# Optimization experiments

Measured on AMD Instinct MI355X. Metric: run time of the kernel, lower is better.

## Reference

```python
import jax, jax.numpy as jnp
import numpy as np

HEADS = 8
DIM_HEAD = 32
EPS = 1e-5


def setup_inputs() -> dict:
    key = jax.random.key(0)
    ks = jax.random.split(key, 12)
    b, dim, H, W = 16, 256, 64, 64
    led = 128
    hid = HEADS * DIM_HEAD
    return {
        "x": jax.random.normal(ks[0], (b, dim, H, W), dtype=jnp.float32),
        "condition": jax.random.normal(ks[1], (b, led), dtype=jnp.float32),
        "w_qkv": jax.random.normal(ks[2], (3 * hid, dim), dtype=jnp.float32) * 0.02,
        "w_lk": jax.random.normal(ks[3], (hid, led), dtype=jnp.float32) * 0.02,
        "b_lk": jax.random.normal(ks[4], (hid,), dtype=jnp.float32) * 0.02,
        "w_lq": jax.random.normal(ks[5], (hid, led), dtype=jnp.float32) * 0.02,
        "b_lq": jax.random.normal(ks[6], (hid,), dtype=jnp.float32) * 0.02,
        "w_out": jax.random.normal(ks[7], (dim, hid), dtype=jnp.float32) * 0.02,
        "b_out": jax.random.normal(ks[8], (dim,), dtype=jnp.float32) * 0.02,
        "gn_gamma": jnp.ones((dim,), dtype=jnp.float32),
        "gn_beta": jnp.zeros((dim,), dtype=jnp.float32),
    }


def reference(x, condition, w_qkv, w_lk, b_lk, w_lq, b_lq, w_out, b_out, gn_gamma, gn_beta):
    b, c, H, W = x.shape
    n = H * W
    scale = DIM_HEAD ** (-0.5)
    hid = HEADS * DIM_HEAD

    # 1x1 conv QKV projection (no bias)
    qkv = jnp.einsum('oc,bchw->bohw', w_qkv, x)  # [b, 3*hid, H, W]
    qkv = qkv.reshape(b, 3, HEADS, DIM_HEAD, n)
    q, k, v = qkv[:, 0], qkv[:, 1], qkv[:, 2]     # each [b, heads, d, n]

    # conditioning biases
    lk = (condition @ w_lk.T + b_lk).reshape(b, HEADS, DIM_HEAD, 1)
    lq = (condition @ w_lq.T + b_lq).reshape(b, HEADS, DIM_HEAD, 1)
    k = k + lk
    q = q + lq

    # double softmax (linear attention)
    q = jax.nn.softmax(q, axis=-2) * scale  # over feature dim d
    k = jax.nn.softmax(k, axis=-1)          # over spatial dim n

    context = jnp.einsum('bhdn,bhen->bhde', k, v)   # [b, h, d, e]
    out = jnp.einsum('bhde,bhdn->bhen', context, q)  # [b, h, e, n]
    out = out.reshape(b, hid, H, W)

    # to_out: 1x1 conv + bias, then GroupNorm(1, dim)
    y = jnp.einsum('oc,bchw->bohw', w_out, out) + b_out[None, :, None, None]
    mean = jnp.mean(y, axis=(1, 2, 3), keepdims=True)
    var = jnp.var(y, axis=(1, 2, 3), keepdims=True)
    y = (y - mean) * jax.lax.rsqrt(var + EPS)
    return y * gn_gamma[None, :, None, None] + gn_beta[None, :, None, None]
```

## Files before the change

kernel.cpp:

```cpp
#include <hip/hip_runtime.h>


#define NB    16
#define DIM   256
#define NSP   4096
#define LED   128
#define HID   256
#define NHEAD 8
#define SCALE 0.17677669529663687f

typedef __bf16 bf16x8 __attribute__((ext_vector_type(8)));
typedef float f32x4 __attribute__((ext_vector_type(4)));
typedef unsigned short us8 __attribute__((ext_vector_type(8)));
typedef unsigned short us4 __attribute__((ext_vector_type(4)));

__device__ __forceinline__ unsigned short f2bf(float f){
  unsigned u = __builtin_bit_cast(unsigned, f);
  u += 0x7fffu + ((u >> 16) & 1u);
  return (unsigned short)(u >> 16);
}
__device__ __forceinline__ float bf2f(unsigned short h){
  unsigned u = ((unsigned)h) << 16;
  return __builtin_bit_cast(float, u);
}
__device__ __forceinline__ bf16x8 ldb8(const unsigned short* p){
  us8 r = *(const us8*)p;
  return __builtin_bit_cast(bf16x8, r);
}
__device__ __forceinline__ f32x4 mfma16(bf16x8 a, bf16x8 b, f32x4 c){
  return __builtin_amdgcn_mfma_f32_16x16x32_bf16(a, b, c, 0, 0, 0);
}
__device__ __forceinline__ void gl16(const unsigned short* g, unsigned short* l){
  __builtin_amdgcn_global_load_lds(
      (const __attribute__((address_space(1))) unsigned int*)g,
      (__attribute__((address_space(3))) unsigned int*)l,
      16, 0, 0);
}

__global__ __launch_bounds__(256) void k0_prep(
    const float* __restrict__ wqkv, const float* __restrict__ cond,
    const float* __restrict__ wlk, const float* __restrict__ blk,
    const float* __restrict__ wlq, const float* __restrict__ blq,
    unsigned short* __restrict__ whi,
    float* __restrict__ lk, float* __restrict__ lq)
{
  const int idx = blockIdx.x*256 + threadIdx.x;
  if (idx < 768*256){
    whi[idx] = f2bf(wqkv[idx]);
  } else {
    int i = idx - 768*256;
    const int which = (i >= NB*HID) ? 1 : 0;
    i &= (NB*HID - 1);
    const int b = i >> 8, o = i & 255;
    const float* wm = which ? wlq : wlk;
    const float* bs = which ? blq : blk;
    float s = bs[o];
    const float* c = cond + b*LED;
    const float* wr = wm + o*LED;
    for (int j=0;j<LED;j++) s += c[j]*wr[j];
    (which ? lq : lk)[i] = s;
  }
}

__global__ __launch_bounds__(256) void k1_txpose(
    const float* __restrict__ x, unsigned short* __restrict__ xt)
{
  __shared__ float tile[64][65];
  const int c0 = blockIdx.x*64, n0 = blockIdx.y*64, b = blockIdx.z;
  const int t = threadIdx.x;
  const int tr = t >> 6, tc = t & 63;
  const float* xp = x + ((size_t)b*DIM + c0)*NSP + n0;
  #pragma unroll
  for (int i=0;i<16;i++){
    const int cl = i*4 + tr;
    tile[cl][tc] = xp[(size_t)cl*NSP + tc];
  }
  __syncthreads();
  unsigned short* xtp = xt + ((size_t)b*NSP + n0)*DIM + c0;
  #pragma unroll
  for (int i=0;i<16;i++){
    const int nl = i*4 + tr;
    xtp[(size_t)nl*DIM + tc] = f2bf(tile[tc][nl]);
  }
}

__global__ __launch_bounds__(256) void k2_gemm1(
    const unsigned short* __restrict__ whi,
    const unsigned short* __restrict__ xt,
    const float* __restrict__ lkv, const float* __restrict__ lqv,
    unsigned short* __restrict__ qh,
    unsigned short* __restrict__ kexp, unsigned short* __restrict__ vout,
    float* __restrict__ ksum)
{
  __shared__ __align__(16) unsigned char smraw[34816];
  unsigned short* Ah  = (unsigned short*)smraw;
  unsigned short* Bt  = (unsigned short*)(smraw + 16384);
  unsigned short* stg = (unsigned short*)smraw;

  const int nt = blockIdx.x, mt = blockIdx.y, b = blockIdx.z;
  const int o0 = mt*128, n0 = nt*128;
  const int t = threadIdx.x, lane = t & 63, wv = t >> 6;
  const int wr = wv >> 1, wc = wv & 1;
  const int cl = lane & 15, g = lane >> 4;

  f32x4 acc[4][4];
  const f32x4 z4 = {0.f,0.f,0.f,0.f};
  #pragma unroll
  for (int m=0;m<4;m++)
    #pragma unroll
    for (int n=0;n<4;n++) acc[m][n] = z4;

  const unsigned short* xb = xt + ((size_t)b*NSP + n0)*DIM;
  const int rowc = lane >> 3;
  const int gcol = 8*((lane & 7) ^ rowc);

  for (int kt=0; kt<4; kt++){
    const int k0 = kt*64;
    __syncthreads();
    #pragma unroll
    for (int j=0;j<4;j++){
      const int rg = wv*4 + j;
      const int rr = rg*8 + rowc;
      gl16(&whi[(size_t)(o0+rr)*DIM + k0 + gcol], &Ah[rg*512]);
      gl16(&xb [(size_t)rr*DIM      + k0 + gcol], &Bt[rg*512]);
    }
    __syncthreads();
    #pragma unroll
    for (int kk=0; kk<2; kk++){
      const int ko = kk*32 + g*8;
      const int kosw = ko ^ ((cl & 7) << 3);
      bf16x8 a1[4], bb[4];
      #pragma unroll
      for (int m=0;m<4;m++){
        const int row = wr*64 + m*16 + cl;
        a1[m] = ldb8(&Ah[row*64 + kosw]);
      }
      #pragma unroll
      for (int n=0;n<4;n++){
        const int row = wc*64 + n*16 + cl;
        bb[n] = ldb8(&Bt[row*64 + kosw]);
      }
      #pragma unroll
      for (int m=0;m<4;m++)
        #pragma unroll
        for (int n=0;n<4;n++)
          acc[m][n] = mfma16(a1[m], bb[n], acc[m][n]);
    }
  }

  __syncthreads();

  if (mt < 2){
    float lqr[4][4];
    #pragma unroll
    for (int m=0;m<4;m++)
      #pragma unroll
      for (int i=0;i<4;i++)
        lqr[m][i] = lqv[b*HID + o0 + wr*64 + m*16 + g*4 + i];
    #pragma unroll
    for (int j=0;j<2;j++){
      #pragma unroll
      for (int nf=0;nf<4;nf++){
        float e[8]; float mx = -1e30f;
        #pragma unroll
        for (int mm=0;mm<2;mm++)
          #pragma unroll
          for (int i=0;i<4;i++){
            const int m = 2*j+mm;
            const float v = acc[m][nf][i] + lqr[m][i];
            e[mm*4+i] = v; mx = fmaxf(mx, v);
          }
        mx = fmaxf(mx, __shfl_xor(mx, 16));
        mx = fmaxf(mx, __shfl_xor(mx, 32));
        float s = 0.f;
        #pragma unroll
        for (int q2=0;q2<8;q2++){ e[q2] = __expf(e[q2]-mx); s += e[q2]; }
        s += __shfl_xor(s, 16);
        s += __shfl_xor(s, 32);
        const float r = 1.f/s;
        const int n_local = wc*64 + nf*16 + cl;
        #pragma unroll
        for (int mm=0;mm<2;mm++){
          const int dg_local = wr*64 + (2*j+mm)*16 + g*4;
          us4 h4;
          #pragma unroll
          for (int i=0;i<4;i++) h4[i] = f2bf(e[mm*4+i]*r);
          *(us4*)&stg[n_local*136 + dg_local] = h4;
        }
      }
    }
    __syncthreads();
    unsigned short* qbase = qh + ((size_t)b*NSP + n0)*HID + o0;
    #pragma unroll
    for (int i2=0;i2<8;i2++){
      const int n_local = wv*32 + i2*4 + (lane>>4);
      const int dg8 = (lane&15)*8;
      us8 val = *(const us8*)&stg[n_local*136 + dg8];
      *(us8*)&qbase[(size_t)n_local*HID + dg8] = val;
    }
  } else {
    const int isK = (mt < 4);
    const int dgbase = isK ? (mt-2)*128 : (mt-4)*128;
    #pragma unroll
    for (int m=0;m<4;m++)
      #pragma unroll
      for (int i=0;i<4;i++){
        const int dg_local = wr*64 + m*16 + g*4 + i;
        const int nb0 = wc*64 + cl;
        if (isK){
          const float lkval = lkv[b*HID + dgbase + dg_local];
          float s = 0.f;
          #pragma unroll
          for (int nf=0;nf<4;nf++){
            const float v = __expf(acc[m][nf][i] + lkval);
            const unsigned short hh = f2bf(v);
            stg[dg_local*136 + nb0 + nf*16] = hh;
            s += bf2f(hh);
          }
          s += __shfl_xor(s,1); s += __shfl_xor(s,2);
          s += __shfl_xor(s,4); s += __shfl_xor(s,8);
          if (cl == 0) atomicAdd(&ksum[b*HID + dgbase + dg_local], s);
        } else {
          #pragma unroll
          for (int nf=0;nf<4;nf++)
            stg[dg_local*136 + nb0 + nf*16] = f2bf(acc[m][nf][i]);
        }
      }
    __syncthreads();
    unsigned short* obase = (isK ? kexp : vout) + ((size_t)b*HID + dgbase)*NSP + n0;
    #pragma unroll
    for (int i2=0;i2<8;i2++){
      const int dg_local = wv*32 + i2*4 + (lane>>4);
      const int n8 = (lane&15)*8;
      us8 val = *(const us8*)&stg[dg_local*136 + n8];
      *(us8*)&obase[(size_t)dg_local*NSP + n8] = val;
    }
  }
}

__global__ __launch_bounds__(256) void k3_ctx(
    const unsigned short* __restrict__ kexp, const unsigned short* __restrict__ vv,
    float* __restrict__ ctxp)
{
  const int half = blockIdx.x, h = blockIdx.y, b = blockIdx.z;
  const int t = threadIdx.x, lane = t&63, wv = t>>6;
  const int cl = lane&15, g = lane>>4;
  const int nstart = half*2048 + wv*512;
  f32x4 acc[2][2];
  const f32x4 z4 = {0.f,0.f,0.f,0.f};
  acc[0][0]=z4; acc[0][1]=z4; acc[1][0]=z4; acc[1][1]=z4;
  const unsigned short* kb = kexp + ((size_t)b*HID + h*32)*NSP;
  const unsigned short* vb = vv   + ((size_t)b*HID + h*32)*NSP;
  for (int ks=0; ks<16; ks++){
    const int k = nstart + ks*32 + g*8;
    bf16x8 a0 = ldb8(&kb[(size_t)(cl)   *NSP + k]);
    bf16x8 a1 = ldb8(&kb[(size_t)(16+cl)*NSP + k]);
    bf16x8 b0 = ldb8(&vb[(size_t)(cl)   *NSP + k]);
    bf16x8 b1 = ldb8(&vb[(size_t)(16+cl)*NSP + k]);
    acc[0][0] = mfma16(a0,b0,acc[0][0]);
    acc[0][1] = mfma16(a0,b1,acc[0][1]);
    acc[1][0] = mfma16(a1,b0,acc[1][0]);
    acc[1][1] = mfma16(a1,b1,acc[1][1]);
  }
  float* outp = ctxp + ((((size_t)b*NHEAD + h)*2 + half)*4 + wv)*1024;
  #pragma unroll
  for (int dm=0;dm<2;dm++)
    #pragma unroll
    for (int em=0;em<2;em++)
      #pragma unroll
      for (int i=0;i<4;i++)
        outp[(dm*16 + g*4 + i)*32 + em*16 + cl] = acc[dm][em][i];
}

__global__ __launch_bounds__(256) void k4_m(
    const float* __restrict__ ctxp, const float* __restrict__ ksum,
    const float* __restrict__ wout,
    unsigned short* __restrict__ mhi, unsigned short* __restrict__ mlo)
{
  const int h = blockIdx.x, b = blockIdx.y;
  __shared__ float ctxl[32][32];
  __shared__ float rkn[32];
  const int t = threadIdx.x;
  const float* base = ctxp + (((size_t)b*NHEAD + h)*8)*1024;
  #pragma unroll
  for (int r=0;r<4;r++){
    const int de = r*256 + t;
    float s = 0.f;
    #pragma unroll
    for (int p=0;p<8;p++) s += base[p*1024 + de];
    ctxl[de>>5][de&31] = s;
  }
  if (t < 32) rkn[t] = SCALE / ksum[b*HID + h*32 + t];
  __syncthreads();
  float w[32];
  const float* wrow = wout + (size_t)t*HID + h*32;
  #pragma unroll
  for (int el=0;el<32;el++) w[el] = wrow[el];
  for (int dl=0; dl<32; dl++){
    float s = 0.f;
    #pragma unroll
    for (int el=0;el<32;el++) s += w[el]*ctxl[dl][el];
    s *= rkn[dl];
    const unsigned short hh = f2bf(s);
    const size_t off = ((size_t)b*HID + t)*HID + h*32 + dl;
    mhi[off] = hh;
    mlo[off] = f2bf(s - bf2f(hh));
  }
}

__global__ __launch_bounds__(256) void k5a_stats(
    const unsigned short* __restrict__ mhi,
    const unsigned short* __restrict__ qhp, const float* __restrict__ bout,
    float* __restrict__ bsum, float* __restrict__ bssq)
{
  __shared__ __align__(16) unsigned char smraw[32768];
  unsigned short* Ah = (unsigned short*)smraw;
  unsigned short* Bh = (unsigned short*)(smraw + 16384);
  __shared__ float red[8];

  const int nt = blockIdx.x, mt = blockIdx.y, b = blockIdx.z;
  const int o0 = mt*128, n0 = nt*128;
  const int t = threadIdx.x, lane = t&63, wv = t>>6;
  const int wr = wv>>1, wc = wv&1;
  const int cl = lane&15, g = lane>>4;

  f32x4 acc[4][4];
  const f32x4 z4 = {0.f,0.f,0.f,0.f};
  #pragma unroll
  for (int m=0;m<4;m++)
    #pragma unroll
    for (int n=0;n<4;n++) acc[m][n] = z4;

  const unsigned short* ab_h = mhi + (size_t)b*HID*HID;
  const unsigned short* bb_h = qhp + ((size_t)b*NSP + n0)*HID;
  const int rowc = lane >> 3;
  const int gcol = 8*((lane & 7) ^ rowc);

  for (int kt=0; kt<4; kt++){
    const int k0 = kt*64;
    __syncthreads();
    #pragma unroll
    for (int j=0;j<4;j++){
      const int rg = wv*4 + j;
      const int rr = rg*8 + rowc;
      gl16(&ab_h[(size_t)(o0+rr)*HID + k0 + gcol], &Ah[rg*512]);
      gl16(&bb_h[(size_t)rr*HID      + k0 + gcol], &Bh[rg*512]);
    }
    __syncthreads();
    #pragma unroll
    for (int kk=0;kk<2;kk++){
      const int ko = kk*32 + g*8;
      const int kosw = ko ^ ((cl & 7) << 3);
      bf16x8 ah[4], bh[4];
      #pragma unroll
      for (int m=0;m<4;m++)
        ah[m] = ldb8(&Ah[(wr*64 + m*16 + cl)*64 + kosw]);
      #pragma unroll
      for (int n=0;n<4;n++)
        bh[n] = ldb8(&Bh[(wc*64 + n*16 + cl)*64 + kosw]);
      #pragma unroll
      for (int m=0;m<4;m++)
        #pragma unroll
        for (int n=0;n<4;n++)
          acc[m][n] = mfma16(ah[m], bh[n], acc[m][n]);
    }
  }

  float lsum = 0.f, lss = 0.f;
  #pragma unroll
  for (int m=0;m<4;m++)
    #pragma unroll
    for (int i=0;i<4;i++){
      const float bo = bout[o0 + wr*64 + m*16 + g*4 + i];
      #pragma unroll
      for (int nf=0;nf<4;nf++){
        const float v = acc[m][nf][i] + bo;
        lsum += v; lss += v*v;
      }
    }
  #pragma unroll
  for (int sft=1; sft<64; sft<<=1){
    lsum += __shfl_xor(lsum, sft);
    lss  += __shfl_xor(lss,  sft);
  }
  if (lane == 0){ red[wv] = lsum; red[4+wv] = lss; }
  __syncthreads();
  if (t == 0){
    atomicAdd(&bsum[b], red[0]+red[1]+red[2]+red[3]);
    atomicAdd(&bssq[b], red[4]+red[5]+red[6]+red[7]);
  }
}

__global__ __launch_bounds__(256) void k5b_write(
    const unsigned short* __restrict__ mhi, const unsigned short* __restrict__ mlo,
    const unsigned short* __restrict__ qhp, const float* __restrict__ bout,
    const float* __restrict__ bsum, const float* __restrict__ bssq,
    const float* __restrict__ gamma, const float* __restrict__ beta,
    float* __restrict__ out)
{
  __shared__ __align__(16) unsigned char smraw[49152];
  unsigned short* Ah = (unsigned short*)smraw;
  unsigned short* Al = (unsigned short*)(smraw + 16384);
  unsigned short* Bh = (unsigned short*)(smraw + 32768);
  float* stg = (float*)smraw;

  const int nt = blockIdx.x, mt = blockIdx.y, b = blockIdx.z;
  const int o0 = mt*128, n0 = nt*128;
  const int t = threadIdx.x, lane = t&63, wv = t>>6;
  const int wr = wv>>1, wc = wv&1;
  const int cl = lane&15, g = lane>>4;

  f32x4 acc[4][4];
  const f32x4 z4 = {0.f,0.f,0.f,0.f};
  #pragma unroll
  for (int m=0;m<4;m++)
    #pragma unroll
    for (int n=0;n<4;n++) acc[m][n] = z4;

  const unsigned short* ab_h = mhi + (size_t)b*HID*HID;
  const unsigned short* ab_l = mlo + (size_t)b*HID*HID;
  const unsigned short* bb_h = qhp + ((size_t)b*NSP + n0)*HID;
  const int rowc = lane >> 3;
  const int gcol = 8*((lane & 7) ^ rowc);

  for (int kt=0; kt<4; kt++){
    const int k0 = kt*64;
    __syncthreads();
    #pragma unroll
    for (int j=0;j<4;j++){
      const int rg = wv*4 + j;
      const int rr = rg*8 + rowc;
      gl16(&ab_h[(size_t)(o0+rr)*HID + k0 + gcol], &Ah[rg*512]);
      gl16(&ab_l[(size_t)(o0+rr)*HID + k0 + gcol], &Al[rg*512]);
      gl16(&bb_h[(size_t)rr*HID      + k0 + gcol], &Bh[rg*512]);
    }
    __syncthreads();
    #pragma unroll
    for (int kk=0;kk<2;kk++){
      const int ko = kk*32 + g*8;
      const int kosw = ko ^ ((cl & 7) << 3);
      bf16x8 ah[4], al[4], bh[4];
      #pragma unroll
      for (int m=0;m<4;m++){
        const int row = wr*64 + m*16 + cl;
        ah[m] = ldb8(&Ah[row*64 + kosw]);
        al[m] = ldb8(&Al[row*64 + kosw]);
      }
      #pragma unroll
      for (int n=0;n<4;n++){
        const int row = wc*64 + n*16 + cl;
        bh[n] = ldb8(&Bh[row*64 + kosw]);
      }
      #pragma unroll
      for (int m=0;m<4;m++)
        #pragma unroll
        for (int n=0;n<4;n++){
          acc[m][n] = mfma16(ah[m], bh[n], acc[m][n]);
          acc[m][n] = mfma16(al[m], bh[n], acc[m][n]);
        }
    }
  }

  const float inv = 1.f/1048576.f;
  const float mean = bsum[b]*inv;
  const float var  = bssq[b]*inv - mean*mean;
  const float ri = rsqrtf(var + 1e-5f);
  float gav[4][4], bev[4][4];
  #pragma unroll
  for (int m=0;m<4;m++)
    #pragma unroll
    for (int i=0;i<4;i++){
      const int o = o0 + wr*64 + m*16 + g*4 + i;
      const float ga = gamma[o]*ri;
      gav[m][i] = ga;
      bev[m][i] = beta[o] + (bout[o]-mean)*ga;
    }

  #pragma unroll
  for (int p=0;p<2;p++){
    __syncthreads();
    #pragma unroll
    for (int mm=0;mm<2;mm++){
      const int m = 2*p+mm;
      #pragma unroll
      for (int nf=0;nf<4;nf++)
        #pragma unroll
        for (int i=0;i<4;i++){
          const int lr = wr*32 + mm*16 + g*4 + i;
          stg[lr*132 + wc*64 + nf*16 + cl] = acc[m][nf][i]*gav[m][i] + bev[m][i];
        }
    }
    __syncthreads();
    #pragma unroll
    for (int i2=0;i2<8;i2++){
      const int lr = wv*16 + i2*2 + (lane>>5);
      const int colw = (lane&31)*4;
      f32x4 v = *(const f32x4*)&stg[lr*132 + colw];
      const int dg = o0 + (lr>>5)*64 + p*32 + (lr&31);
      *(f32x4*)&out[((size_t)b*HID + dg)*NSP + n0 + colw] = v;
    }
  }
}

#define OFF_XT     0ull
#define OFF_QH     33554432ull
#define OFF_CTXP   100663296ull
#define OFF_MH     104857600ull
#define OFF_ML     106954752ull
#define OFF_LK     109051904ull
#define OFF_LQ     109068288ull
#define OFF_WHI    109084672ull
#define OFF_KSUM   109871104ull
#define OFF_BSUM   109887488ull
#define OFF_BSSQ   109887552ull

extern "C" void kernel_launch(void* const* d_in, const int* in_sizes, int n_in,
                              void* d_out, int out_size, void* d_ws, size_t ws_size,
                              hipStream_t stream) {
  const float* x     = (const float*)d_in[0];
  const float* cond  = (const float*)d_in[1];
  const float* wqkv  = (const float*)d_in[2];
  const float* wlk   = (const float*)d_in[3];
  const float* blk   = (const float*)d_in[4];
  const float* wlq   = (const float*)d_in[5];
  const float* blq   = (const float*)d_in[6];
  const float* wout  = (const float*)d_in[7];
  const float* bout  = (const float*)d_in[8];
  const float* gamma = (const float*)d_in[9];
  const float* beta  = (const float*)d_in[10];

  char* ws = (char*)d_ws;
  unsigned short* xt   = (unsigned short*)(ws + OFF_XT);
  unsigned short* qh   = (unsigned short*)(ws + OFF_QH);
  float*          ctxp = (float*)(ws + OFF_CTXP);
  unsigned short* mhi  = (unsigned short*)(ws + OFF_MH);
  unsigned short* mlo  = (unsigned short*)(ws + OFF_ML);
  float*          lk   = (float*)(ws + OFF_LK);
  float*          lq   = (float*)(ws + OFF_LQ);
  unsigned short* whi  = (unsigned short*)(ws + OFF_WHI);
  float*          ksum = (float*)(ws + OFF_KSUM);
  float*          bsum = (float*)(ws + OFF_BSUM);
  float*          bssq = (float*)(ws + OFF_BSSQ);

  unsigned short* kexp = (unsigned short*)d_out;
  unsigned short* vscr = (unsigned short*)d_out + 16777216;
  float*          y    = (float*)d_out;

  hipMemsetAsync(ws + OFF_KSUM, 0, 16384 + 128, stream);

  k0_prep  <<<800, 256, 0, stream>>>(wqkv, cond, wlk, blk, wlq, blq, whi, lk, lq);
  k1_txpose<<<dim3(4,64,16), 256, 0, stream>>>(x, xt);
  k2_gemm1 <<<dim3(32,6,16), 256, 0, stream>>>(whi, xt, lk, lq, qh, kexp, vscr, ksum);
  k3_ctx   <<<dim3(2,8,16), 256, 0, stream>>>(kexp, vscr, ctxp);
  k4_m     <<<dim3(8,16), 256, 0, stream>>>(ctxp, ksum, wout, mhi, mlo);
  k5a_stats<<<dim3(32,2,16), 256, 0, stream>>>(mhi, qh, bout, bsum, bssq);
  k5b_write<<<dim3(32,2,16), 256, 0, stream>>>(mhi, mlo, qh, bout, bsum, bssq, gamma, beta, y);
}
```

Before: 163.9 us.

## Fuse K/V projection with context GEMM to avoid materializing exp(K) and V

The QKV GEMM kernel and the context kernel are merged. Each 512-thread block now computes two 128-row panels: Q panels as before, or a matching K panel and V panel for four heads. exp(K) and V stay in shared memory and are reduced straight into per-tile context partials, so the bf16 K and V tensors are no longer written to and read back from global memory. In exchange, k4 must sum 32 partials per head instead of 8, and the block uses about 68KB of LDS with extra syncs, which lowers occupancy.

```diff
diff --git a/kernel.cpp b/kernel.cpp
--- a/kernel.cpp
+++ b/kernel.cpp
@@ -84,91 +84,90 @@
   }
 }
 
-__global__ __launch_bounds__(256) void k2_gemm1(
+__global__ __launch_bounds__(512) void k2_fused(
     const unsigned short* __restrict__ whi,
     const unsigned short* __restrict__ xt,
     const float* __restrict__ lkv, const float* __restrict__ lqv,
     unsigned short* __restrict__ qh,
-    unsigned short* __restrict__ kexp, unsigned short* __restrict__ vout,
-    float* __restrict__ ksum)
+    float* __restrict__ ksum, float* __restrict__ ctxp)
 {
-  __shared__ __align__(16) unsigned char smraw[34816];
-  unsigned short* Ah  = (unsigned short*)smraw;
-  unsigned short* Bt  = (unsigned short*)(smraw + 16384);
-  unsigned short* stg = (unsigned short*)smraw;
-
-  const int nt = blockIdx.x, mt = blockIdx.y, b = blockIdx.z;
-  const int o0 = mt*128, n0 = nt*128;
+  __shared__ __align__(16) unsigned char smraw[68608];
+  unsigned short* Abuf = (unsigned short*)smraw;
+  unsigned short* Bbuf = (unsigned short*)(smraw + 16384);
+  unsigned short* Ubuf = (unsigned short*)(smraw + 32768);
+
+  const int nt = blockIdx.x, type = blockIdx.y, b = blockIdx.z;
+  const int n0 = nt*128;
   const int t = threadIdx.x, lane = t & 63, wv = t >> 6;
   const int wr = wv >> 1, wc = wv & 1;
   const int cl = lane & 15, g = lane >> 4;
 
-  f32x4 acc[4][4];
-  const f32x4 z4 = {0.f,0.f,0.f,0.f};
-  #pragma unroll
-  for (int m=0;m<4;m++)
-    #pragma unroll
-    for (int n=0;n<4;n++) acc[m][n] = z4;
-
   const unsigned short* xb = xt + ((size_t)b*NSP + n0)*DIM;
   const int rowc = lane >> 3;
   const int gcol = 8*((lane & 7) ^ rowc);
 
-  for (int kt=0; kt<4; kt++){
-    const int k0 = kt*64;
-    __syncthreads();
-    #pragma unroll
-    for (int j=0;j<4;j++){
-      const int rg = wv*4 + j;
-      const int rr = rg*8 + rowc;
-      gl16(&whi[(size_t)(o0+rr)*DIM + k0 + gcol], &Ah[rg*512]);
-      gl16(&xb [(size_t)rr*DIM      + k0 + gcol], &Bt[rg*512]);
-    }
-    __syncthreads();
-    #pragma unroll
-    for (int kk=0; kk<2; kk++){
-      const int ko = kk*32 + g*8;
-      const int kosw = ko ^ ((cl & 7) << 3);
-      bf16x8 a1[4], bb[4];
-      #pragma unroll
-      for (int m=0;m<4;m++){
-        const int row = wr*64 + m*16 + cl;
-        a1[m] = ldb8(&Ah[row*64 + kosw]);
-      }
-      #pragma unroll
-      for (int n=0;n<4;n++){
-        const int row = wc*64 + n*16 + cl;
-        bb[n] = ldb8(&Bt[row*64 + kosw]);
-      }
-      #pragma unroll
-      for (int m=0;m<4;m++)
+  f32x4 ctxacc[2];
+  ctxacc[0] = (f32x4){0.f,0.f,0.f,0.f};
+  ctxacc[1] = (f32x4){0.f,0.f,0.f,0.f};
+
+  for (int panel=0; panel<2; ++panel){
+    const int prow = (type==0) ? panel*128
+                   : (type==1) ? (panel ? 512 : 256)
+                               : (panel ? 640 : 384);
+    f32x4 acc[2][4];
+    const f32x4 z4 = {0.f,0.f,0.f,0.f};
+    #pragma unroll
+    for (int m=0;m<2;m++)
+      #pragma unroll
+      for (int n=0;n<4;n++) acc[m][n] = z4;
+
+    for (int kt=0; kt<4; kt++){
+      const int k0 = kt*64;
+      __syncthreads();
+      #pragma unroll
+      for (int j=0;j<2;j++){
+        const int rg = wv*2 + j;
+        const int rr = rg*8 + rowc;
+        gl16(&whi[(size_t)(prow+rr)*DIM + k0 + gcol], &Abuf[rg*512]);
+        gl16(&xb [(size_t)rr*DIM       + k0 + gcol], &Bbuf[rg*512]);
+      }
+      __syncthreads();
+      #pragma unroll
+      for (int kk=0; kk<2; kk++){
+        const int ko = kk*32 + g*8;
+        const int kosw = ko ^ ((cl & 7) << 3);
+        bf16x8 a[2], bfr[4];
+        #pragma unroll
+        for (int m=0;m<2;m++)
+          a[m] = ldb8(&Abuf[(wr*32 + m*16 + cl)*64 + kosw]);
         #pragma unroll
         for (int n=0;n<4;n++)
-          acc[m][n] = mfma16(a1[m], bb[n], acc[m][n]);
-    }
-  }
-
-  __syncthreads();
-
-  if (mt < 2){
-    float lqr[4][4];
-    #pragma unroll
-    for (int m=0;m<4;m++)
-      #pragma unroll
-      for (int i=0;i<4;i++)
-        lqr[m][i] = lqv[b*HID + o0 + wr*64 + m*16 + g*4 + i];
-    #pragma unroll
-    for (int j=0;j<2;j++){
+          bfr[n] = ldb8(&Bbuf[(wc*64 + n*16 + cl)*64 + kosw]);
+        #pragma unroll
+        for (int m=0;m<2;m++)
+          #pragma unroll
+          for (int n=0;n<4;n++)
+            acc[m][n] = mfma16(a[m], bfr[n], acc[m][n]);
+      }
+    }
+    __syncthreads();
+
+    if (type == 0){
+      float lqr[2][4];
+      #pragma unroll
+      for (int m=0;m<2;m++)
+        #pragma unroll
+        for (int i=0;i<4;i++)
+          lqr[m][i] = lqv[b*HID + panel*128 + wr*32 + m*16 + g*4 + i];
       #pragma unroll
       for (int nf=0;nf<4;nf++){
         float e[8]; float mx = -1e30f;
         #pragma unroll
-        for (int mm=0;mm<2;mm++)
+        for (int m=0;m<2;m++)
           #pragma unroll
           for (int i=0;i<4;i++){
-            const int m = 2*j+mm;
             const float v = acc[m][nf][i] + lqr[m][i];
-            e[mm*4+i] = v; mx = fmaxf(mx, v);
+            e[m*4+i] = v; mx = fmaxf(mx, v);
           }
         mx = fmaxf(mx, __shfl_xor(mx, 16));
         mx = fmaxf(mx, __shfl_xor(mx, 32));
@@ -180,96 +179,84 @@
         const float r = 1.f/s;
         const int n_local = wc*64 + nf*16 + cl;
         #pragma unroll
-        for (int mm=0;mm<2;mm++){
-          const int dg_local = wr*64 + (2*j+mm)*16 + g*4;
+        for (int m=0;m<2;m++){
+          const int dg_local = wr*32 + m*16 + g*4;
           us4 h4;
           #pragma unroll
-          for (int i=0;i<4;i++) h4[i] = f2bf(e[mm*4+i]*r);
-          *(us4*)&stg[n_local*136 + dg_local] = h4;
+          for (int i=0;i<4;i++) h4[i] = f2bf(e[m*4+i]*r);
+          *(us4*)&Ubuf[n_local*140 + dg_local] = h4;
         }
       }
-    }
-    __syncthreads();
-    unsigned short* qbase = qh + ((size_t)b*NSP + n0)*HID + o0;
-    #pragma unroll
-    for (int i2=0;i2<8;i2++){
-      const int n_local = wv*32 + i2*4 + (lane>>4);
-      const int dg8 = (lane&15)*8;
-      us8 val = *(const us8*)&stg[n_local*136 + dg8];
-      *(us8*)&qbase[(size_t)n_local*HID + dg8] = val;
-    }
-  } else {
-    const int isK = (mt < 4);
-    const int dgbase = isK ? (mt-2)*128 : (mt-4)*128;
-    #pragma unroll
-    for (int m=0;m<4;m++)
-      #pragma unroll
-      for (int i=0;i<4;i++){
-        const int dg_local = wr*64 + m*16 + g*4 + i;
-        const int nb0 = wc*64 + cl;
-        if (isK){
-          const float lkval = lkv[b*HID + dgbase + dg_local];
+      __syncthreads();
+      unsigned short* qbase = qh + ((size_t)b*NSP + n0)*HID + panel*128;
+      #pragma unroll
+      for (int i2=0;i2<4;i2++){
+        const int n_local = i2*32 + (t>>4);
+        const int dg8 = (t&15)*8;
+        us8 val = *(const us8*)&Ubuf[n_local*140 + dg8];
+        *(us8*)&qbase[(size_t)n_local*HID + dg8] = val;
+      }
+    } else if (panel == 0){
+      const int dgk = (type-1)*128;
+      #pragma unroll
+      for (int m=0;m<2;m++)
+        #pragma unroll
+        for (int i=0;i<4;i++){
+          const int row = wr*32 + m*16 + g*4 + i;
+          const float lkval = lkv[b*HID + dgk + row];
           float s = 0.f;
           #pragma unroll
           for (int nf=0;nf<4;nf++){
             const float v = __expf(acc[m][nf][i] + lkval);
             const unsigned short hh = f2bf(v);
-            stg[dg_local*136 + nb0 + nf*16] = hh;
+            const int col = nf*16 + cl;
+            Ubuf[wc*8192 + row*64 + (col ^ ((row&7)<<3))] = hh;
             s += bf2f(hh);
           }
           s += __shfl_xor(s,1); s += __shfl_xor(s,2);
           s += __shfl_xor(s,4); s += __shfl_xor(s,8);
-          if (cl == 0) atomicAdd(&ksum[b*HID + dgbase + dg_local], s);
-        } else {
+          if (cl == 0) atomicAdd(&ksum[b*HID + dgk + row], s);
+        }
+    } else {
+      const int hl = wv >> 1, e16 = wv & 1;
+      #pragma unroll
+      for (int half=0; half<2; half++){
+        __syncthreads();
+        if (wc == half){
           #pragma unroll
-          for (int nf=0;nf<4;nf++)
-            stg[dg_local*136 + nb0 + nf*16] = f2bf(acc[m][nf][i]);
+          for (int m=0;m<2;m++)
+            #pragma unroll
+            for (int i=0;i<4;i++){
+              const int row = wr*32 + m*16 + g*4 + i;
+              #pragma unroll
+              for (int nf=0;nf<4;nf++){
+                const int col = nf*16 + cl;
+                Bbuf[row*64 + (col ^ ((row&7)<<3))] = f2bf(acc[m][nf][i]);
+              }
+            }
         }
-      }
-    __syncthreads();
-    unsigned short* obase = (isK ? kexp : vout) + ((size_t)b*HID + dgbase)*NSP + n0;
-    #pragma unroll
-    for (int i2=0;i2<8;i2++){
-      const int dg_local = wv*32 + i2*4 + (lane>>4);
-      const int n8 = (lane&15)*8;
-      us8 val = *(const us8*)&stg[dg_local*136 + n8];
-      *(us8*)&obase[(size_t)dg_local*NSP + n8] = val;
-    }
-  }
-}
-
-__global__ __launch_bounds__(256) void k3_ctx(
-    const unsigned short* __restrict__ kexp, const unsigned short* __restrict__ vv,
-    float* __restrict__ ctxp)
-{
-  const int half = blockIdx.x, h = blockIdx.y, b = blockIdx.z;
-  const int t = threadIdx.x, lane = t&63, wv = t>>6;
-  const int cl = lane&15, g = lane>>4;
-  const int nstart = half*2048 + wv*512;
-  f32x4 acc[2][2];
-  const f32x4 z4 = {0.f,0.f,0.f,0.f};
-  acc[0][0]=z4; acc[0][1]=z4; acc[1][0]=z4; acc[1][1]=z4;
-  const unsigned short* kb = kexp + ((size_t)b*HID + h*32)*NSP;
-  const unsigned short* vb = vv   + ((size_t)b*HID + h*32)*NSP;
-  for (int ks=0; ks<16; ks++){
-    const int k = nstart + ks*32 + g*8;
-    bf16x8 a0 = ldb8(&kb[(size_t)(cl)   *NSP + k]);
-    bf16x8 a1 = ldb8(&kb[(size_t)(16+cl)*NSP + k]);
-    bf16x8 b0 = ldb8(&vb[(size_t)(cl)   *NSP + k]);
-    bf16x8 b1 = ldb8(&vb[(size_t)(16+cl)*NSP + k]);
-    acc[0][0] = mfma16(a0,b0,acc[0][0]);
-    acc[0][1] = mfma16(a0,b1,acc[0][1]);
-    acc[1][0] = mfma16(a1,b0,acc[1][0]);
-    acc[1][1] = mfma16(a1,b1,acc[1][1]);
-  }
-  float* outp = ctxp + ((((size_t)b*NHEAD + h)*2 + half)*4 + wv)*1024;
-  #pragma unroll
-  for (int dm=0;dm<2;dm++)
-    #pragma unroll
-    for (int em=0;em<2;em++)
-      #pragma unroll
-      for (int i=0;i<4;i++)
-        outp[(dm*16 + g*4 + i)*32 + em*16 + cl] = acc[dm][em][i];
+        __syncthreads();
+        #pragma unroll
+        for (int d16=0; d16<2; d16++){
+          #pragma unroll
+          for (int ks=0; ks<2; ks++){
+            const int ko = ks*32 + g*8;
+            const int kosw = ko ^ ((cl & 7) << 3);
+            bf16x8 af = ldb8(&Ubuf[half*8192 + (hl*32 + d16*16 + cl)*64 + kosw]);
+            bf16x8 bf = ldb8(&Bbuf[(hl*32 + e16*16 + cl)*64 + kosw]);
+            ctxacc[d16] = mfma16(af, bf, ctxacc[d16]);
+          }
+        }
+      }
+      const int hg = (type-1)*4 + hl;
+      float* base = ctxp + (((size_t)(b*NHEAD + hg)*32 + nt)*1024);
+      #pragma unroll
+      for (int d16=0; d16<2; d16++)
+        #pragma unroll
+        for (int i=0;i<4;i++)
+          base[(d16*16 + g*4 + i)*32 + e16*16 + cl] = ctxacc[d16][i];
+    }
+  }
 }
 
 __global__ __launch_bounds__(256) void k4_m(
@@ -281,15 +268,11 @@
   __shared__ float ctxl[32][32];
   __shared__ float rkn[32];
   const int t = threadIdx.x;
-  const float* base = ctxp + (((size_t)b*NHEAD + h)*8)*1024;
-  #pragma unroll
-  for (int r=0;r<4;r++){
-    const int de = r*256 + t;
-    float s = 0.f;
-    #pragma unroll
-    for (int p=0;p<8;p++) s += base[p*1024 + de];
-    ctxl[de>>5][de&31] = s;
-  }
+  const float* base = ctxp + ((size_t)(b*NHEAD + h)*32)*1024;
+  f32x4 sacc = {0.f,0.f,0.f,0.f};
+  for (int nt=0; nt<32; nt++)
+    sacc += *(const f32x4*)&base[nt*1024 + t*4];
+  *(f32x4*)&((float*)ctxl)[t*4] = sacc;
   if (t < 32) rkn[t] = SCALE / ksum[b*HID + h*32 + t];
   __syncthreads();
   float w[32];
@@ -504,15 +487,15 @@
 
 #define OFF_XT     0ull
 #define OFF_QH     33554432ull
-#define OFF_CTXP   100663296ull
-#define OFF_MH     104857600ull
-#define OFF_ML     106954752ull
-#define OFF_LK     109051904ull
-#define OFF_LQ     109068288ull
-#define OFF_WHI    109084672ull
-#define OFF_KSUM   109871104ull
-#define OFF_BSUM   109887488ull
-#define OFF_BSSQ   109887552ull
+#define OFF_CTXP   67108864ull
+#define OFF_MH     83886080ull
+#define OFF_ML     85983232ull
+#define OFF_LK     88080384ull
+#define OFF_LQ     88096768ull
+#define OFF_WHI    88113152ull
+#define OFF_KSUM   88506368ull
+#define OFF_BSUM   88522752ull
+#define OFF_BSSQ   88522816ull
 
 extern "C" void kernel_launch(void* const* d_in, const int* in_sizes, int n_in,
                               void* d_out, int out_size, void* d_ws, size_t ws_size,
@@ -542,16 +525,13 @@
   float*          bsum = (float*)(ws + OFF_BSUM);
   float*          bssq = (float*)(ws + OFF_BSSQ);
 
-  unsigned short* kexp = (unsigned short*)d_out;
-  unsigned short* vscr = (unsigned short*)d_out + 16777216;
-  float*          y    = (float*)d_out;
+  float* y = (float*)d_out;
 
   hipMemsetAsync(ws + OFF_KSUM, 0, 16384 + 128, stream);
 
   k0_prep  <<<800, 256, 0, stream>>>(wqkv, cond, wlk, blk, wlq, blq, whi, lk, lq);
   k1_txpose<<<dim3(4,64,16), 256, 0, stream>>>(x, xt);
-  k2_gemm1 <<<dim3(32,6,16), 256, 0, stream>>>(whi, xt, lk, lq, qh, kexp, vscr, ksum);
-  k3_ctx   <<<dim3(2,8,16), 256, 0, stream>>>(kexp, vscr, ctxp);
+  k2_fused <<<dim3(32,3,16), 512, 0, stream>>>(whi, xt, lk, lq, qh, ksum, ctxp);
   k4_m     <<<dim3(8,16), 256, 0, stream>>>(ctxp, ksum, wout, mhi, mlo);
   k5a_stats<<<dim3(32,2,16), 256, 0, stream>>>(mhi, qh, bout, bsum, bssq);
   k5b_write<<<dim3(32,2,16), 256, 0, stream>>>(mhi, mlo, qh, bout, bsum, bssq, gamma, beta, y);
```

Result: slower. 178.2 us (+8.7%).
